# Kernel optimization log

Hardware: AMD Instinct MI355X
Metric: run time of the kernel (lower is better)

The kernel has to match this reference:

```python
import jax, jax.numpy as jnp
import numpy as np

C = 256
CQK = C // 8


def setup_inputs() -> dict:
    key = jax.random.key(0)
    ks = jax.random.split(key, 8)
    B, H, W = 4, 64, 64
    inputs = jax.random.normal(ks[0], (B, H, W, C), dtype=jnp.float32)
    s = 1.0 / np.sqrt(C)
    Wq = jax.random.normal(ks[1], (C, CQK), dtype=jnp.float32) * s
    bq = jnp.zeros((CQK,), dtype=jnp.float32)
    Wk = jax.random.normal(ks[2], (C, CQK), dtype=jnp.float32) * s
    bk = jnp.zeros((CQK,), dtype=jnp.float32)
    Wv = jax.random.normal(ks[3], (C, C), dtype=jnp.float32) * s
    bv = jnp.zeros((C,), dtype=jnp.float32)
    gamma = jnp.float32(0.7)  # nonzero so attention branch contributes
    return {"inputs": inputs, "Wq": Wq, "bq": bq, "Wk": Wk, "bk": bk,
            "Wv": Wv, "bv": bv, "gamma": gamma}


def reference(inputs, Wq, bq, Wk, bk, Wv, bv, gamma):
    B, H, W, Cin = inputs.shape
    N = H * W
    x = inputs.reshape(B, N, Cin)
    # 1x1 convs == per-pixel channel matmuls
    q = x @ Wq + bq                      # (B, N, C//8)
    k = x @ Wk + bk                      # (B, N, C//8)
    v = x @ Wv + bv                      # (B, N, C)
    energy = jnp.einsum('bnd,bmd->bnm', q, k)   # (B, N, N), no scale (faithful)
    attn = jax.nn.softmax(energy, axis=-1)
    x_out = jnp.einsum('bnm,bmc->bnc', attn, v)  # (B, N, C)
    out = gamma * x_out.reshape(B, H, W, Cin) + inputs
    return out
```

## Files before the change

kernel.cpp:

```cpp
#include <hip/hip_runtime.h>
#include <hip/hip_bf16.h>

#define B_ 4
#define N_ 4096
#define C_ 256
#define D_ 32
#define LOG2E 1.44269504088896340736f
#define MFMA16 __builtin_amdgcn_mfma_f32_16x16x32_bf16

typedef __attribute__((ext_vector_type(8))) short short8;
typedef __attribute__((ext_vector_type(4))) short short4v;
typedef __attribute__((ext_vector_type(4))) float float4v;

__device__ inline short f2bf_rne(float f) {
  unsigned u = __builtin_bit_cast(unsigned, f);
  u += 0x7FFFu + ((u >> 16) & 1u);
  return (short)(u >> 16);
}
__device__ inline float bf2f(short s) {
  unsigned u = ((unsigned)(unsigned short)s) << 16;
  return __builtin_bit_cast(float, u);
}
__device__ inline float fast_exp2(float x) { return __builtin_amdgcn_exp2f(x); }

__global__ __launch_bounds__(256) void cast_w_kernel(
    const float* __restrict__ Wq, const float* __restrict__ Wk,
    const float* __restrict__ Wv, short* __restrict__ WtF) {
  int i  = blockIdx.x * 256 + threadIdx.x;
  int j  = i & 7;
  int l  = (i >> 3) & 63;
  int ks = (i >> 9) & 7;
  int nb = i >> 12;
  int n  = nb * 16 + (l & 15);
  int k  = ks * 32 + ((l >> 4) << 3) + j;
  float v;
  if (n < 32)      v = Wq[k * 32 + n] * LOG2E;
  else if (n < 64) v = Wk[k * 32 + (n - 32)];
  else             v = Wv[k * 256 + (n - 64)];
  WtF[i] = f2bf_rne(v);
}

__global__ __launch_bounds__(256, 4) void proj_kernel(
    const float* __restrict__ x, const short* __restrict__ WtF,
    const float* __restrict__ bq, const float* __restrict__ bk,
    const float* __restrict__ bv,
    short* __restrict__ qb, short* __restrict__ kF, short* __restrict__ vF) {
  int blk = blockIdx.x;
  int b  = blk >> 7;
  int r0 = (blk & 127) * 32;
  int t  = threadIdx.x;
  int w  = t >> 6;
  int l  = t & 63;
  int lc = l & 15;
  int q4 = l >> 4;

  __shared__ __align__(16) short sA[32][272];
  __shared__ __align__(16) short sV[256][40];
  __shared__ __align__(16) short sK[32][36];

  {
    const float* xb = x + (size_t)(b * N_ + r0) * C_;
#pragma unroll
    for (int ch = 0; ch < 8; ch++) {
      int f   = ch * 256 + t;
      int row = f >> 6;
      int col = (f & 63) * 4;
      float4v v = *(const float4v*)(xb + f * 4);
      short4v s;
      s[0] = f2bf_rne(v[0]); s[1] = f2bf_rne(v[1]);
      s[2] = f2bf_rne(v[2]); s[3] = f2bf_rne(v[3]);
      *(short4v*)(&sA[row][col]) = s;
    }
  }
  __syncthreads();

  float4v acc[10];
#pragma unroll
  for (int i = 0; i < 10; i++) { acc[i][0] = 0.f; acc[i][1] = 0.f; acc[i][2] = 0.f; acc[i][3] = 0.f; }

#pragma unroll
  for (int ks = 0; ks < 8; ks++) {
    short8 af0 = *(const short8*)(&sA[lc][ks * 32 + q4 * 8]);
    short8 af1 = *(const short8*)(&sA[16 + lc][ks * 32 + q4 * 8]);
#pragma unroll
    for (int nbo = 0; nbo < 5; nbo++) {
      int nb = nbo * 4 + w;
      short8 bf = *(const short8*)(WtF + (((nb << 3) + ks) << 9) + l * 8);
      acc[nbo * 2 + 0] = MFMA16(af0, bf, acc[nbo * 2 + 0], 0, 0, 0);
      acc[nbo * 2 + 1] = MFMA16(af1, bf, acc[nbo * 2 + 1], 0, 0, 0);
    }
  }

#pragma unroll
  for (int nbo = 0; nbo < 5; nbo++) {
    float bias;
    if (nbo == 0) bias = (w < 2) ? bq[w * 16 + lc] * LOG2E : bk[(w - 2) * 16 + lc];
    else          bias = bv[(nbo - 1) * 64 + w * 16 + lc];
#pragma unroll
    for (int rt = 0; rt < 2; rt++) {
#pragma unroll
      for (int r = 0; r < 4; r++) {
        int row = rt * 16 + q4 * 4 + r;
        short s = f2bf_rne(acc[nbo * 2 + rt][r] + bias);
        if (nbo == 0) {
          if (w < 2) qb[(size_t)(b * N_ + r0 + row) * D_ + w * 16 + lc] = s;
          else       sK[row][(w - 2) * 16 + lc] = s;
        } else {
          sV[(nbo - 1) * 64 + w * 16 + lc][row] = s;
        }
      }
    }
  }
  __syncthreads();

  int kt  = r0 >> 6;
  int ks0 = (r0 >> 5) & 1;

  {
    int c = t;
    size_t tb = ((size_t)(b * 64 + kt) * 32 + ks0 * 16 + (c >> 4)) * 512;
#pragma unroll
    for (int rg = 0; rg < 4; rg++) {
      short8 vv = *(const short8*)(&sV[c][rg * 8]);
      *(short8*)(vF + tb + (rg * 16 + (c & 15)) * 8) = vv;
    }
  }
  if (t < 128) {
    int row = t >> 2, dg = t & 3;
    size_t tb = ((size_t)(b * 64 + kt) * 4 + ks0 * 2 + (row >> 4)) * 512;
    short8 kv = *(const short8*)(&sK[row][dg * 8]);
    *(short8*)(kF + tb + (dg * 16 + (row & 15)) * 8) = kv;
  }
}

__global__ __launch_bounds__(512, 4) void flash_partial_kernel(
    const short* __restrict__ qb, const short* __restrict__ kF,
    const short* __restrict__ vF, short* __restrict__ obuf,
    float* __restrict__ lbuf) {
  int blk = blockIdx.x;
  int b  = blk & 3;
  int hb = (blk >> 2) & 1;
  int qt = blk >> 3;
  int r0 = qt * 64;
  int t  = threadIdx.x;
  int w  = t >> 6;
  int l  = t & 63;
  int lc = l & 15;
  int q4 = l >> 4;
  int rq = w & 3;
  bool qkw = (w < 4);

  __shared__ __align__(16) short sP[2][64][72];

  int p = (b * 64 + qt) * 2 + hb;

  short8 qf = *(const short8*)(qb + (size_t)(b * N_ + r0 + rq * 16 + lc) * D_ + q4 * 8);

  const short* kbp = kF + ((size_t)(b * 64 + hb * 32) * 4) * 512 + l * 8;
  const short* vbp = vF + ((size_t)(b * 64 + hb * 32) * 32 + 2 * w) * 512 + l * 8;

  short8 kC0, kC1, kC2, kC3;
  short8 vX00, vX01, vX10, vX11;
  short8 vY00, vY01, vY10, vY11;

  kC0 = *(const short8*)(kbp + 0);
  kC1 = *(const short8*)(kbp + 512);
  kC2 = *(const short8*)(kbp + 1024);
  kC3 = *(const short8*)(kbp + 1536);
  vX00 = *(const short8*)(vbp + 0);
  vX01 = *(const short8*)(vbp + 512);
  vX10 = *(const short8*)(vbp + 8192);
  vX11 = *(const short8*)(vbp + 8704);

  float4v O[8];
#pragma unroll
  for (int i = 0; i < 8; i++) { O[i][0] = 0.f; O[i][1] = 0.f; O[i][2] = 0.f; O[i][3] = 0.f; }
  float l_part = 0.f;

#define K_RELOAD(TI)                                                           \
  { size_t o_ = (size_t)(TI) * 2048;                                           \
    kC0 = *(const short8*)(kbp + o_);                                          \
    kC1 = *(const short8*)(kbp + o_ + 512);                                    \
    kC2 = *(const short8*)(kbp + o_ + 1024);                                   \
    kC3 = *(const short8*)(kbp + o_ + 1536); }

#define QK_STEP(SPB, VALID)                                                    \
  { float4v z; z[0] = 0.f; z[1] = 0.f; z[2] = 0.f; z[3] = 0.f;                 \
    float4v S0 = MFMA16(kC0, qf, z, 0, 0, 0);                                  \
    float4v S1 = MFMA16(kC1, qf, z, 0, 0, 0);                                  \
    float4v S2 = MFMA16(kC2, qf, z, 0, 0, 0);                                  \
    float4v S3 = MFMA16(kC3, qf, z, 0, 0, 0);                                  \
    short* rowp = &sP[SPB][rq * 16 + lc][q4 * 4];                              \
    float ts = 0.f;                                                            \
    { float p0 = fast_exp2(S0[0]), p1 = fast_exp2(S0[1]);                      \
      float p2 = fast_exp2(S0[2]), p3 = fast_exp2(S0[3]);                      \
      ts += (p0 + p1) + (p2 + p3);                                             \
      short4v pk; pk[0] = f2bf_rne(p0); pk[1] = f2bf_rne(p1);                  \
      pk[2] = f2bf_rne(p2); pk[3] = f2bf_rne(p3);                              \
      *(short4v*)(rowp + 0) = pk; }                                            \
    { float p0 = fast_exp2(S1[0]), p1 = fast_exp2(S1[1]);                      \
      float p2 = fast_exp2(S1[2]), p3 = fast_exp2(S1[3]);                      \
      ts += (p0 + p1) + (p2 + p3);                                             \
      short4v pk; pk[0] = f2bf_rne(p0); pk[1] = f2bf_rne(p1);                  \
      pk[2] = f2bf_rne(p2); pk[3] = f2bf_rne(p3);                              \
      *(short4v*)(rowp + 16) = pk; }                                           \
    { float p0 = fast_exp2(S2[0]), p1 = fast_exp2(S2[1]);                      \
      float p2 = fast_exp2(S2[2]), p3 = fast_exp2(S2[3]);                      \
      ts += (p0 + p1) + (p2 + p3);                                             \
      short4v pk; pk[0] = f2bf_rne(p0); pk[1] = f2bf_rne(p1);                  \
      pk[2] = f2bf_rne(p2); pk[3] = f2bf_rne(p3);                              \
      *(short4v*)(rowp + 32) = pk; }                                           \
    { float p0 = fast_exp2(S3[0]), p1 = fast_exp2(S3[1]);                      \
      float p2 = fast_exp2(S3[2]), p3 = fast_exp2(S3[3]);                      \
      ts += (p0 + p1) + (p2 + p3);                                             \
      short4v pk; pk[0] = f2bf_rne(p0); pk[1] = f2bf_rne(p1);                  \
      pk[2] = f2bf_rne(p2); pk[3] = f2bf_rne(p3);                              \
      *(short4v*)(rowp + 48) = pk; }                                           \
    if (VALID) l_part += ts; }

#define PV_STEP(SPB, V00, V01, V10, V11)                                       \
  { _Pragma("unroll")                                                          \
    for (int rt = 0; rt < 4; rt++) {                                           \
      short8 pf0 = *(const short8*)(&sP[SPB][rt * 16 + lc][q4 * 8]);           \
      short8 pf1 = *(const short8*)(&sP[SPB][rt * 16 + lc][32 + q4 * 8]);      \
      O[rt * 2 + 0] = MFMA16(pf0, V00, O[rt * 2 + 0], 0, 0, 0);                \
      O[rt * 2 + 0] = MFMA16(pf1, V10, O[rt * 2 + 0], 0, 0, 0);                \
      O[rt * 2 + 1] = MFMA16(pf0, V01, O[rt * 2 + 1], 0, 0, 0);                \
      O[rt * 2 + 1] = MFMA16(pf1, V11, O[rt * 2 + 1], 0, 0, 0);                \
    } }

  if (qkw) {
    QK_STEP(0, true)
    K_RELOAD(1)
  }
  __syncthreads();

  for (int ti = 0; ti < 32; ti += 2) {
    int n1 = ti + 1;
    int n2 = (ti + 2 < 32) ? ti + 2 : 31;
    bool v2 = (ti + 2 < 32);
    int n3 = (ti + 3 < 32) ? ti + 3 : 31;

    { size_t vo = (size_t)n1 * 16384;
      vY00 = *(const short8*)(vbp + vo);
      vY01 = *(const short8*)(vbp + vo + 512);
      vY10 = *(const short8*)(vbp + vo + 8192);
      vY11 = *(const short8*)(vbp + vo + 8704); }
    if (qkw) {
      QK_STEP(1, true)
      K_RELOAD(n2)
    }
    PV_STEP(0, vX00, vX01, vX10, vX11)
    __syncthreads();

    { size_t vo = (size_t)n2 * 16384;
      vX00 = *(const short8*)(vbp + vo);
      vX01 = *(const short8*)(vbp + vo + 512);
      vX10 = *(const short8*)(vbp + vo + 8192);
      vX11 = *(const short8*)(vbp + vo + 8704); }
    if (qkw) {
      QK_STEP(0, v2)
      K_RELOAD(n3)
    }
    PV_STEP(1, vY00, vY01, vY10, vY11)
    __syncthreads();
  }
#undef K_RELOAD
#undef QK_STEP
#undef PV_STEP

  {
    short* ob = obuf + ((size_t)p * 64 + w * 8) * 256 + l * 4;
#pragma unroll
    for (int a = 0; a < 8; a++) {
      float4v o = O[a];
      short4v pk;
      pk[0] = f2bf_rne(o[0]); pk[1] = f2bf_rne(o[1]);
      pk[2] = f2bf_rne(o[2]); pk[3] = f2bf_rne(o[3]);
      *(short4v*)(ob + a * 256) = pk;
    }
  }
  if (qkw) {
    float l_tot = l_part + __shfl_xor(l_part, 16, 64);
    l_tot += __shfl_xor(l_tot, 32, 64);
    if (q4 == 0) lbuf[(size_t)p * 64 + rq * 16 + lc] = l_tot;
  }
}

__global__ __launch_bounds__(256) void merge_kernel(
    const short* __restrict__ obuf, const float* __restrict__ lbuf,
    const float* __restrict__ xin, const float* __restrict__ gptr,
    float* __restrict__ out) {
  int blk = blockIdx.x;
  int t   = threadIdx.x;
  int s   = t >> 2;
  int qr  = t & 3;
  int wv  = s >> 3, j = s & 7, rt = j >> 1, cbo = j & 1;
  int chb = wv * 32 + cbo * 16;
  float g = *gptr;

  const short* o0 = obuf + ((size_t)(blk * 2 + 0) * 64 + s) * 256 + qr * 64;
  const short* o1 = obuf + ((size_t)(blk * 2 + 1) * 64 + s) * 256 + qr * 64;
  const float* l0 = lbuf + (size_t)(blk * 2 + 0) * 64;
  const float* l1 = lbuf + (size_t)(blk * 2 + 1) * 64;

  short4v a[16], c[16];
#pragma unroll
  for (int i = 0; i < 16; i++) {
    a[i] = ((const short4v*)o0)[i];
    c[i] = ((const short4v*)o1)[i];
  }

  size_t rowbase = (size_t)blk * 64;
#pragma unroll
  for (int r = 0; r < 4; r++) {
    int q = rt * 16 + qr * 4 + r;
    float linv = __builtin_amdgcn_rcpf(l0[q] + l1[q]);
    size_t gi = (rowbase + q) * C_ + chb;
#pragma unroll
    for (int i0 = 0; i0 < 16; i0 += 4) {
      float4v xv = *(const float4v*)(xin + gi + i0);
      float4v ov;
#pragma unroll
      for (int e = 0; e < 4; e++)
        ov[e] = g * ((bf2f(a[i0 + e][r]) + bf2f(c[i0 + e][r])) * linv) + xv[e];
      *(float4v*)(out + gi + i0) = ov;
    }
  }
}

extern "C" void kernel_launch(void* const* d_in, const int* in_sizes, int n_in,
                              void* d_out, int out_size, void* d_ws, size_t ws_size,
                              hipStream_t stream) {
  const float* x     = (const float*)d_in[0];
  const float* Wq    = (const float*)d_in[1];
  const float* bq    = (const float*)d_in[2];
  const float* Wk    = (const float*)d_in[3];
  const float* bk    = (const float*)d_in[4];
  const float* Wv    = (const float*)d_in[5];
  const float* bv    = (const float*)d_in[6];
  const float* gamma = (const float*)d_in[7];
  float* out = (float*)d_out;

  char* ws = (char*)d_ws;
  short* qb   = (short*)ws;
  short* kF   = (short*)(ws + (1u << 20));
  short* vF   = (short*)(ws + (2u << 20));
  short* WtF  = (short*)(ws + (10u << 20));
  short* obuf = (short*)(ws + (11u << 20));
  float* lbuf = (float*)(ws + (28u << 20));

  hipLaunchKernelGGL(cast_w_kernel,        dim3(320), dim3(256), 0, stream, Wq, Wk, Wv, WtF);
  hipLaunchKernelGGL(proj_kernel,          dim3(512), dim3(256), 0, stream, x, WtF, bq, bk, bv, qb, kF, vF);
  hipLaunchKernelGGL(flash_partial_kernel, dim3(512), dim3(512), 0, stream, qb, kF, vF, obuf, lbuf);
  hipLaunchKernelGGL(merge_kernel,         dim3(256), dim3(256), 0, stream, obuf, lbuf, x, gamma, out);
}
```

Baseline: 147.7 us.

## Fuse split-K merge into flash kernel via atomic counter; pipeline projection weight loads

Removes the separate merge kernel. The second of the two key-half blocks for each query tile, detected with an atomic counter, combines its in-register output with the partner's bf16 partial and writes the residual output directly. The projection kernel now double-buffers its weight fragment loads and writes V and K tiles with more contiguous, vectorised stores. This saves one launch and one round trip of the partials through memory, at the cost of a memset, threadfences and an uneven tail where only half the blocks do the merge.

```diff
diff --git a/kernel.cpp b/kernel.cpp
--- a/kernel.cpp
+++ b/kernel.cpp
@@ -78,38 +78,74 @@
 #pragma unroll
   for (int i = 0; i < 10; i++) { acc[i][0] = 0.f; acc[i][1] = 0.f; acc[i][2] = 0.f; acc[i][3] = 0.f; }
 
-#pragma unroll
-  for (int ks = 0; ks < 8; ks++) {
-    short8 af0 = *(const short8*)(&sA[lc][ks * 32 + q4 * 8]);
-    short8 af1 = *(const short8*)(&sA[16 + lc][ks * 32 + q4 * 8]);
-#pragma unroll
-    for (int nbo = 0; nbo < 5; nbo++) {
-      int nb = nbo * 4 + w;
-      short8 bf = *(const short8*)(WtF + (((nb << 3) + ks) << 9) + l * 8);
-      acc[nbo * 2 + 0] = MFMA16(af0, bf, acc[nbo * 2 + 0], 0, 0, 0);
-      acc[nbo * 2 + 1] = MFMA16(af1, bf, acc[nbo * 2 + 1], 0, 0, 0);
-    }
-  }
-
-#pragma unroll
-  for (int nbo = 0; nbo < 5; nbo++) {
-    float bias;
-    if (nbo == 0) bias = (w < 2) ? bq[w * 16 + lc] * LOG2E : bk[(w - 2) * 16 + lc];
-    else          bias = bv[(nbo - 1) * 64 + w * 16 + lc];
+  const short* wbase = WtF + w * 4096 + l * 8;
+
+#define LOADW(B0, B1, B2, B3, B4, KS)                       \
+  B0 = *(const short8*)(wbase + (KS) * 512 + 0 * 16384);    \
+  B1 = *(const short8*)(wbase + (KS) * 512 + 1 * 16384);    \
+  B2 = *(const short8*)(wbase + (KS) * 512 + 2 * 16384);    \
+  B3 = *(const short8*)(wbase + (KS) * 512 + 3 * 16384);    \
+  B4 = *(const short8*)(wbase + (KS) * 512 + 4 * 16384);
+
+#define DO_MFMA(A0, A1, B0, B1, B2, B3, B4)                 \
+  acc[0] = MFMA16(A0, B0, acc[0], 0, 0, 0);                 \
+  acc[1] = MFMA16(A1, B0, acc[1], 0, 0, 0);                 \
+  acc[2] = MFMA16(A0, B1, acc[2], 0, 0, 0);                 \
+  acc[3] = MFMA16(A1, B1, acc[3], 0, 0, 0);                 \
+  acc[4] = MFMA16(A0, B2, acc[4], 0, 0, 0);                 \
+  acc[5] = MFMA16(A1, B2, acc[5], 0, 0, 0);                 \
+  acc[6] = MFMA16(A0, B3, acc[6], 0, 0, 0);                 \
+  acc[7] = MFMA16(A1, B3, acc[7], 0, 0, 0);                 \
+  acc[8] = MFMA16(A0, B4, acc[8], 0, 0, 0);                 \
+  acc[9] = MFMA16(A1, B4, acc[9], 0, 0, 0);
+
+  short8 wA0, wA1, wA2, wA3, wA4, wB0, wB1, wB2, wB3, wB4;
+  LOADW(wA0, wA1, wA2, wA3, wA4, 0)
+#pragma unroll
+  for (int kk = 0; kk < 8; kk += 2) {
+    short8 a00 = *(const short8*)(&sA[lc][kk * 32 + q4 * 8]);
+    short8 a01 = *(const short8*)(&sA[16 + lc][kk * 32 + q4 * 8]);
+    LOADW(wB0, wB1, wB2, wB3, wB4, kk + 1)
+    DO_MFMA(a00, a01, wA0, wA1, wA2, wA3, wA4)
+    short8 a10 = *(const short8*)(&sA[lc][(kk + 1) * 32 + q4 * 8]);
+    short8 a11 = *(const short8*)(&sA[16 + lc][(kk + 1) * 32 + q4 * 8]);
+    LOADW(wA0, wA1, wA2, wA3, wA4, kk + 2)
+    DO_MFMA(a10, a11, wB0, wB1, wB2, wB3, wB4)
+  }
+#undef LOADW
+#undef DO_MFMA
+
+  {
+    float bias0 = (w < 2) ? bq[w * 16 + lc] * LOG2E : bk[(w - 2) * 16 + lc];
 #pragma unroll
     for (int rt = 0; rt < 2; rt++) {
-#pragma unroll
-      for (int r = 0; r < 4; r++) {
-        int row = rt * 16 + q4 * 4 + r;
-        short s = f2bf_rne(acc[nbo * 2 + rt][r] + bias);
-        if (nbo == 0) {
-          if (w < 2) qb[(size_t)(b * N_ + r0 + row) * D_ + w * 16 + lc] = s;
-          else       sK[row][(w - 2) * 16 + lc] = s;
-        } else {
-          sV[(nbo - 1) * 64 + w * 16 + lc][row] = s;
+      if (w < 2) {
+#pragma unroll
+        for (int r = 0; r < 4; r++) {
+          int row = rt * 16 + q4 * 4 + r;
+          qb[(size_t)(b * N_ + r0 + row) * D_ + w * 16 + lc] =
+              f2bf_rne(acc[rt][r] + bias0);
+        }
+      } else {
+#pragma unroll
+        for (int r = 0; r < 4; r++) {
+          int row = rt * 16 + q4 * 4 + r;
+          sK[row][(w - 2) * 16 + lc] = f2bf_rne(acc[rt][r] + bias0);
         }
       }
     }
+#pragma unroll
+    for (int nbo = 1; nbo < 5; nbo++) {
+      float bias = bv[(nbo - 1) * 64 + w * 16 + lc];
+#pragma unroll
+      for (int rt = 0; rt < 2; rt++) {
+        float4v a = acc[nbo * 2 + rt];
+        short4v pk;
+        pk[0] = f2bf_rne(a[0] + bias); pk[1] = f2bf_rne(a[1] + bias);
+        pk[2] = f2bf_rne(a[2] + bias); pk[3] = f2bf_rne(a[3] + bias);
+        *(short4v*)(&sV[(nbo - 1) * 64 + w * 16 + lc][rt * 16 + q4 * 4]) = pk;
+      }
+    }
   }
   __syncthreads();
 
@@ -117,26 +153,31 @@
   int ks0 = (r0 >> 5) & 1;
 
   {
-    int c = t;
-    size_t tb = ((size_t)(b * 64 + kt) * 32 + ks0 * 16 + (c >> 4)) * 512;
-#pragma unroll
-    for (int rg = 0; rg < 4; rg++) {
-      short8 vv = *(const short8*)(&sV[c][rg * 8]);
-      *(short8*)(vF + tb + (rg * 16 + (c & 15)) * 8) = vv;
+    size_t tb2 = ((size_t)(b * 64 + kt) * 32 + ks0 * 16) * 512;
+    int cb = t >> 4;
+#pragma unroll
+    for (int k = 0; k < 4; k++) {
+      int p = (t & 15) * 4 + k;
+      int j = p >> 4, i = p & 15;
+      short8 vv = *(const short8*)(&sV[cb * 16 + i][j * 8]);
+      *(short8*)(vF + tb2 + (size_t)t * 32 + k * 8) = vv;
     }
   }
   if (t < 128) {
-    int row = t >> 2, dg = t & 3;
-    size_t tb = ((size_t)(b * 64 + kt) * 4 + ks0 * 2 + (row >> 4)) * 512;
-    short8 kv = *(const short8*)(&sK[row][dg * 8]);
-    *(short8*)(kF + tb + (dg * 16 + (row & 15)) * 8) = kv;
-  }
-}
-
-__global__ __launch_bounds__(512, 4) void flash_partial_kernel(
+    int fr = t >> 6, ll = t & 63;
+    int kv = fr * 16 + (ll & 15), dg = ll >> 4;
+    size_t tbk = ((size_t)(b * 64 + kt) * 4 + ks0 * 2) * 512;
+    short8 kv8 = *(const short8*)(&sK[kv][dg * 8]);
+    *(short8*)(kF + tbk + (size_t)t * 8) = kv8;
+  }
+}
+
+__global__ __launch_bounds__(512, 4) void flash_kernel(
     const short* __restrict__ qb, const short* __restrict__ kF,
     const short* __restrict__ vF, short* __restrict__ obuf,
-    float* __restrict__ lbuf) {
+    float* __restrict__ lbuf, int* __restrict__ cnt,
+    const float* __restrict__ xin, const float* __restrict__ gptr,
+    float* __restrict__ out) {
   int blk = blockIdx.x;
   int b  = blk & 3;
   int hb = (blk >> 2) & 1;
@@ -151,8 +192,12 @@
   bool qkw = (w < 4);
 
   __shared__ __align__(16) short sP[2][64][72];
-
-  int p = (b * 64 + qt) * 2 + hb;
+  __shared__ float sL[64];
+  __shared__ int sFlag;
+
+  int pidx = b * 64 + qt;
+  int po   = pidx * 2 + hb;
+  int pp   = pidx * 2 + (1 - hb);
 
   short8 qf = *(const short8*)(qb + (size_t)(b * N_ + r0 + rq * 16 + lc) * D_ + q4 * 8);
 
@@ -270,7 +315,7 @@
 #undef PV_STEP
 
   {
-    short* ob = obuf + ((size_t)p * 64 + w * 8) * 256 + l * 4;
+    short* ob = obuf + ((size_t)po * 64 + w * 8) * 256 + l * 4;
 #pragma unroll
     for (int a = 0; a < 8; a++) {
       float4v o = O[a];
@@ -283,48 +328,42 @@
   if (qkw) {
     float l_tot = l_part + __shfl_xor(l_part, 16, 64);
     l_tot += __shfl_xor(l_tot, 32, 64);
-    if (q4 == 0) lbuf[(size_t)p * 64 + rq * 16 + lc] = l_tot;
-  }
-}
-
-__global__ __launch_bounds__(256) void merge_kernel(
-    const short* __restrict__ obuf, const float* __restrict__ lbuf,
-    const float* __restrict__ xin, const float* __restrict__ gptr,
-    float* __restrict__ out) {
-  int blk = blockIdx.x;
-  int t   = threadIdx.x;
-  int s   = t >> 2;
-  int qr  = t & 3;
-  int wv  = s >> 3, j = s & 7, rt = j >> 1, cbo = j & 1;
-  int chb = wv * 32 + cbo * 16;
-  float g = *gptr;
-
-  const short* o0 = obuf + ((size_t)(blk * 2 + 0) * 64 + s) * 256 + qr * 64;
-  const short* o1 = obuf + ((size_t)(blk * 2 + 1) * 64 + s) * 256 + qr * 64;
-  const float* l0 = lbuf + (size_t)(blk * 2 + 0) * 64;
-  const float* l1 = lbuf + (size_t)(blk * 2 + 1) * 64;
-
-  short4v a[16], c[16];
-#pragma unroll
-  for (int i = 0; i < 16; i++) {
-    a[i] = ((const short4v*)o0)[i];
-    c[i] = ((const short4v*)o1)[i];
-  }
-
-  size_t rowbase = (size_t)blk * 64;
-#pragma unroll
-  for (int r = 0; r < 4; r++) {
-    int q = rt * 16 + qr * 4 + r;
-    float linv = __builtin_amdgcn_rcpf(l0[q] + l1[q]);
-    size_t gi = (rowbase + q) * C_ + chb;
-#pragma unroll
-    for (int i0 = 0; i0 < 16; i0 += 4) {
-      float4v xv = *(const float4v*)(xin + gi + i0);
-      float4v ov;
-#pragma unroll
-      for (int e = 0; e < 4; e++)
-        ov[e] = g * ((bf2f(a[i0 + e][r]) + bf2f(c[i0 + e][r])) * linv) + xv[e];
-      *(float4v*)(out + gi + i0) = ov;
+    if (q4 == 0) {
+      lbuf[(size_t)po * 64 + rq * 16 + lc] = l_tot;
+      sL[rq * 16 + lc] = l_tot;
+    }
+  }
+  __syncthreads();
+
+  if (t == 0) {
+    __threadfence();
+    int old = atomicAdd(&cnt[pidx], 1);
+    sFlag = (old == 1);
+  }
+  __syncthreads();
+
+  if (sFlag) {
+    __threadfence();
+    const short* pb = obuf + ((size_t)pp * 64 + w * 8) * 256 + l * 4;
+    const float* lp = lbuf + (size_t)pp * 64;
+    short4v pa[8];
+#pragma unroll
+    for (int a = 0; a < 8; a++) pa[a] = *(const short4v*)(pb + a * 256);
+    float g = *gptr;
+#pragma unroll
+    for (int rt = 0; rt < 4; rt++) {
+#pragma unroll
+      for (int r = 0; r < 4; r++) {
+        int q = rt * 16 + q4 * 4 + r;
+        float linv = __builtin_amdgcn_rcpf(sL[q] + lp[q]);
+        size_t base = (size_t)(b * N_ + r0 + q) * C_ + w * 32;
+#pragma unroll
+        for (int cbo = 0; cbo < 2; cbo++) {
+          int a = rt * 2 + cbo;
+          size_t idx = base + cbo * 16 + lc;
+          out[idx] = g * ((O[a][r] + bf2f(pa[a][r])) * linv) + xin[idx];
+        }
+      }
     }
   }
 }
@@ -349,9 +388,11 @@
   short* WtF  = (short*)(ws + (10u << 20));
   short* obuf = (short*)(ws + (11u << 20));
   float* lbuf = (float*)(ws + (28u << 20));
-
-  hipLaunchKernelGGL(cast_w_kernel,        dim3(320), dim3(256), 0, stream, Wq, Wk, Wv, WtF);
-  hipLaunchKernelGGL(proj_kernel,          dim3(512), dim3(256), 0, stream, x, WtF, bq, bk, bv, qb, kF, vF);
-  hipLaunchKernelGGL(flash_partial_kernel, dim3(512), dim3(512), 0, stream, qb, kF, vF, obuf, lbuf);
-  hipLaunchKernelGGL(merge_kernel,         dim3(256), dim3(256), 0, stream, obuf, lbuf, x, gamma, out);
-}
+  int*   cnt  = (int*)(ws + (28u << 20) + (192u << 10));
+
+  hipMemsetAsync(cnt, 0, 256 * sizeof(int), stream);
+  hipLaunchKernelGGL(cast_w_kernel, dim3(320), dim3(256), 0, stream, Wq, Wk, Wv, WtF);
+  hipLaunchKernelGGL(proj_kernel,   dim3(512), dim3(256), 0, stream, x, WtF, bq, bk, bv, qb, kF, vF);
+  hipLaunchKernelGGL(flash_kernel,  dim3(512), dim3(512), 0, stream, qb, kF, vF,
+                     obuf, lbuf, cnt, x, gamma, out);
+}
```

After: 222.4 us. 50.5% more time.
